# Kernel optimization log

Hardware: AMD Instinct MI355X
Metric: run time of the kernel (lower is better)

The kernel has to match this reference:

```python
import jax, jax.numpy as jnp
import numpy as np

NEG_SLOPE = 0.2

def setup_inputs() -> dict:
    key = jax.random.key(0)
    k1, k2, k3 = jax.random.split(key, 3)
    B, C, H, W = 8, 256, 128, 128
    R = 16  # reduction -> squeeze dim C // R = 16
    Cs = C // R
    x = jax.random.normal(k1, (B, C, H, W), dtype=jnp.float32)
    w1 = jax.random.normal(k2, (Cs, C), dtype=jnp.float32) * (1.0 / np.sqrt(C))
    b1 = jnp.zeros((Cs,), dtype=jnp.float32)
    w2 = jax.random.normal(k3, (C, Cs), dtype=jnp.float32) * (1.0 / np.sqrt(Cs))
    b2 = jnp.zeros((C,), dtype=jnp.float32)
    return {"x": x, "w1": w1, "b1": b1, "w2": w2, "b2": b2}

def reference(x, w1, b1, w2, b2):
    # Global average pool over spatial dims: [B,C,H,W] -> [B,C]
    y = jnp.mean(x, axis=(2, 3))
    # 1x1 conv on [B,C,1,1] == GEMV: squeeze + LeakyReLU(0.2)
    y1 = jnp.einsum('bc,sc->bs', y, w1) + b1
    y1 = jnp.where(y1 >= 0, y1, NEG_SLOPE * y1)
    # excite + sigmoid gate
    y2 = jax.nn.sigmoid(jnp.einsum('bs,cs->bc', y1, w2) + b2)
    # broadcast channel-wise scale
    return x * y2[:, :, None, None]
```

## Files before the change

### kernel.cpp

```cpp
#include <hip/hip_runtime.h>
#include <math.h>


#define Bn 8
#define Cn 256
#define CSn 16
#define HWn 16384
#define HW4 4096
#define NEG_SLOPE 0.2f

__global__ __launch_bounds__(256) void pool_kernel(const float* __restrict__ x,
                                                   float* __restrict__ y) {
    const int bc = blockIdx.x;
    const float4* xp = (const float4*)(x + (size_t)bc * HWn);
    float sum = 0.f;
    #pragma unroll
    for (int i = 0; i < HW4 / 256; ++i) {
        float4 v = xp[threadIdx.x + i * 256];
        sum += (v.x + v.y) + (v.z + v.w);
    }
    #pragma unroll
    for (int off = 32; off > 0; off >>= 1)
        sum += __shfl_down(sum, off, 64);
    __shared__ float smem[4];
    const int lane = threadIdx.x & 63, wid = threadIdx.x >> 6;
    if (lane == 0) smem[wid] = sum;
    __syncthreads();
    if (threadIdx.x == 0) {
        float t = (smem[0] + smem[1]) + (smem[2] + smem[3]);
        y[bc] = t * (1.0f / (float)HWn);
    }
}

__global__ __launch_bounds__(256) void gate_kernel(const float* __restrict__ y,
                                                   const float* __restrict__ w1,
                                                   const float* __restrict__ b1,
                                                   const float* __restrict__ w2,
                                                   const float* __restrict__ b2,
                                                   float* __restrict__ y2) {
    __shared__ float y1s[Bn * CSn];
    const int t = threadIdx.x;
    if (t < Bn * CSn) {
        const int b = t / CSn, s = t % CSn;
        float acc = b1[s];
        const float* yb = y + b * Cn;
        const float* ws = w1 + s * Cn;
        #pragma unroll 8
        for (int c = 0; c < Cn; ++c) acc += yb[c] * ws[c];
        y1s[t] = (acc >= 0.f) ? acc : NEG_SLOPE * acc;
    }
    __syncthreads();
    const int c = t;
    const float* w2c = w2 + c * CSn;
    float bias = b2[c];
    #pragma unroll
    for (int b = 0; b < Bn; ++b) {
        float acc = bias;
        #pragma unroll
        for (int s = 0; s < CSn; ++s) acc += y1s[b * CSn + s] * w2c[s];
        y2[b * Cn + c] = 1.0f / (1.0f + __expf(-acc));
    }
}

__global__ __launch_bounds__(256) void scale_kernel(const float* __restrict__ x,
                                                    const float* __restrict__ y2,
                                                    float* __restrict__ out) {
    const size_t i = (size_t)blockIdx.x * 256 + threadIdx.x;
    const int bc = (int)(i >> 12);
    const float g = y2[bc];
    float4 v = ((const float4*)x)[i];
    v.x *= g; v.y *= g; v.z *= g; v.w *= g;
    ((float4*)out)[i] = v;
}

extern "C" void kernel_launch(void* const* d_in, const int* in_sizes, int n_in,
                              void* d_out, int out_size, void* d_ws, size_t ws_size,
                              hipStream_t stream) {
    const float* x  = (const float*)d_in[0];
    const float* w1 = (const float*)d_in[1];
    const float* b1 = (const float*)d_in[2];
    const float* w2 = (const float*)d_in[3];
    const float* b2 = (const float*)d_in[4];
    float* out = (float*)d_out;

    float* y  = (float*)d_ws;
    float* y2 = (float*)d_ws + Bn * Cn;

    pool_kernel<<<Bn * Cn, 256, 0, stream>>>(x, y);
    gate_kernel<<<1, 256, 0, stream>>>(y, w1, b1, w2, b2, y2);
    scale_kernel<<<(Bn * Cn * HWn / 4) / 256, 256, 0, stream>>>(x, y2, out);
}
```

Measured before the change: 265.8 us.

## Fuse pool, gate and scale into one cooperative kernel with grid sync

Replaces the three separate launches with one cooperative kernel of 1024 blocks. Each block pools two channel planes, then waits at a grid-wide sync. It then recomputes its batch's squeeze GEMV locally and scales the same two planes it just read, hoping to hit cache on the re-read. This removes two launch boundaries and the single-block gate kernel. In exchange it adds a grid barrier, redundant squeeze work in every block, and depends on all blocks being co-resident.

```diff
diff --git a/kernel.cpp b/kernel.cpp
--- a/kernel.cpp
+++ b/kernel.cpp
@@ -1,76 +1,94 @@
 #include <hip/hip_runtime.h>
+#include <hip/hip_cooperative_groups.h>
 #include <math.h>
 
+namespace cg = cooperative_groups;
 
 #define Bn 8
 #define Cn 256
 #define CSn 16
 #define HWn 16384
-#define HW4 4096
+#define PL4 4096
 #define NEG_SLOPE 0.2f
+#define NBLK 1024
 
-__global__ __launch_bounds__(256) void pool_kernel(const float* __restrict__ x,
-                                                   float* __restrict__ y) {
-    const int bc = blockIdx.x;
-    const float4* xp = (const float4*)(x + (size_t)bc * HWn);
-    float sum = 0.f;
-    #pragma unroll
-    for (int i = 0; i < HW4 / 256; ++i) {
-        float4 v = xp[threadIdx.x + i * 256];
-        sum += (v.x + v.y) + (v.z + v.w);
+__global__ __launch_bounds__(256, 4) void fused_kernel(
+    const float* __restrict__ x,  const float* __restrict__ w1,
+    const float* __restrict__ b1, const float* __restrict__ w2,
+    const float* __restrict__ b2, float* __restrict__ out,
+    float* __restrict__ y) {
+    const int t = threadIdx.x;
+    const int bc0 = blockIdx.x * 2;
+    const float4* p0 = (const float4*)x + (size_t)bc0 * PL4;
+    const float4* p1 = p0 + PL4;
+
+    float s0 = 0.f, s1 = 0.f;
+    #pragma unroll 4
+    for (int i = 0; i < PL4 / 256; ++i) {
+        float4 a = p0[t + i * 256];
+        float4 b = p1[t + i * 256];
+        s0 += (a.x + a.y) + (a.z + a.w);
+        s1 += (b.x + b.y) + (b.z + b.w);
     }
     #pragma unroll
-    for (int off = 32; off > 0; off >>= 1)
-        sum += __shfl_down(sum, off, 64);
-    __shared__ float smem[4];
-    const int lane = threadIdx.x & 63, wid = threadIdx.x >> 6;
-    if (lane == 0) smem[wid] = sum;
+    for (int off = 32; off; off >>= 1) {
+        s0 += __shfl_down(s0, off, 64);
+        s1 += __shfl_down(s1, off, 64);
+    }
+    __shared__ float sm0[4], sm1[4];
+    const int lane = t & 63, wid = t >> 6;
+    if (lane == 0) { sm0[wid] = s0; sm1[wid] = s1; }
     __syncthreads();
-    if (threadIdx.x == 0) {
-        float t = (smem[0] + smem[1]) + (smem[2] + smem[3]);
-        y[bc] = t * (1.0f / (float)HWn);
+    if (t == 0) {
+        y[bc0]     = (sm0[0] + sm0[1] + sm0[2] + sm0[3]) * (1.f / (float)HWn);
+        y[bc0 + 1] = (sm1[0] + sm1[1] + sm1[2] + sm1[3]) * (1.f / (float)HWn);
+        __threadfence();
     }
-}
 
-__global__ __launch_bounds__(256) void gate_kernel(const float* __restrict__ y,
-                                                   const float* __restrict__ w1,
-                                                   const float* __restrict__ b1,
-                                                   const float* __restrict__ w2,
-                                                   const float* __restrict__ b2,
-                                                   float* __restrict__ y2) {
-    __shared__ float y1s[Bn * CSn];
-    const int t = threadIdx.x;
-    if (t < Bn * CSn) {
-        const int b = t / CSn, s = t % CSn;
-        float acc = b1[s];
-        const float* yb = y + b * Cn;
-        const float* ws = w1 + s * Cn;
-        #pragma unroll 8
-        for (int c = 0; c < Cn; ++c) acc += yb[c] * ws[c];
+    cg::this_grid().sync();
+
+    const int b = bc0 >> 8;
+    __shared__ float part[16 * 17];
+    __shared__ float y1s[16];
+    __shared__ float gv[2];
+    {
+        const int s = t >> 4, j = t & 15;
+        const float* yb = y  + b * Cn + j * 16;
+        const float* wr = w1 + s * Cn + j * 16;
+        float p = 0.f;
+        #pragma unroll
+        for (int k = 0; k < 16; ++k) p += yb[k] * wr[k];
+        part[s * 17 + j] = p;
+    }
+    __syncthreads();
+    if (t < 16) {
+        float acc = b1[t];
+        #pragma unroll
+        for (int j = 0; j < 16; ++j) acc += part[t * 17 + j];
         y1s[t] = (acc >= 0.f) ? acc : NEG_SLOPE * acc;
     }
     __syncthreads();
-    const int c = t;
-    const float* w2c = w2 + c * CSn;
-    float bias = b2[c];
-    #pragma unroll
-    for (int b = 0; b < Bn; ++b) {
-        float acc = bias;
+    if (t < 2) {
+        const int c = (bc0 + t) & (Cn - 1);
+        float acc = b2[c];
         #pragma unroll
-        for (int s = 0; s < CSn; ++s) acc += y1s[b * CSn + s] * w2c[s];
-        y2[b * Cn + c] = 1.0f / (1.0f + __expf(-acc));
+        for (int s = 0; s < CSn; ++s) acc += y1s[s] * w2[c * CSn + s];
+        gv[t] = 1.f / (1.f + __expf(-acc));
     }
-}
+    __syncthreads();
+    const float g0 = gv[0], g1 = gv[1];
 
-__global__ __launch_bounds__(256) void scale_kernel(const float* __restrict__ x,
-                                                    const float* __restrict__ y2,
-                                                    float* __restrict__ out) {
-    const size_t i = (size_t)blockIdx.x * 256 + threadIdx.x;
-    const int bc = (int)(i >> 12);
-    const float g = y2[bc];
-    float4 v = ((const float4*)x)[i];
-    v.x *= g; v.y *= g; v.z *= g; v.w *= g;
-    ((float4*)out)[i] = v;
+    float4* o0 = (float4*)out + (size_t)bc0 * PL4;
+    float4* o1 = o0 + PL4;
+    #pragma unroll 4
+    for (int i = 0; i < PL4 / 256; ++i) {
+        float4 a  = p0[t + i * 256];
+        float4 b4 = p1[t + i * 256];
+        a.x *= g0;  a.y *= g0;  a.z *= g0;  a.w *= g0;
+        b4.x *= g1; b4.y *= g1; b4.z *= g1; b4.w *= g1;
+        o0[t + i * 256] = a;
+        o1[t + i * 256] = b4;
+    }
 }
 
 extern "C" void kernel_launch(void* const* d_in, const int* in_sizes, int n_in,
@@ -82,11 +100,10 @@
     const float* w2 = (const float*)d_in[3];
     const float* b2 = (const float*)d_in[4];
     float* out = (float*)d_out;
+    float* y   = (float*)d_ws;
 
-    float* y  = (float*)d_ws;
-    float* y2 = (float*)d_ws + Bn * Cn;
-
-    pool_kernel<<<Bn * Cn, 256, 0, stream>>>(x, y);
-    gate_kernel<<<1, 256, 0, stream>>>(y, w1, b1, w2, b2, y2);
-    scale_kernel<<<(Bn * Cn * HWn / 4) / 256, 256, 0, stream>>>(x, y2, out);
+    void* args[] = {(void*)&x, (void*)&w1, (void*)&b1, (void*)&w2,
+                    (void*)&b2, (void*)&out, (void*)&y};
+    hipLaunchCooperativeKernel((void*)fused_kernel, dim3(NBLK), dim3(256),
+                               args, 0, stream);
 }
```

Measured after the change: 413.5 us. 1.56x slower.

## Fuse gate computation into scale kernel with per-channel blocks and nontemporal stores

Applied to the files above, without the earlier changes.

Removes the single-block gate kernel and instead has each scale block, one per (batch, channel) plane, recompute the squeeze GEMV, LeakyReLU and its own sigmoid gate from the pooled means. The scale kernel now loops over a full 16384-element plane per block and writes the output with nontemporal stores. This drops one launch and the serial one-block gate stage, at the cost of redundant small GEMV work in every block and fewer, larger blocks.

```diff
diff --git a/kernel.cpp b/kernel.cpp
--- a/kernel.cpp
+++ b/kernel.cpp
@@ -1,76 +1,84 @@
 #include <hip/hip_runtime.h>
 #include <math.h>
-
 
 #define Bn 8
 #define Cn 256
 #define CSn 16
 #define HWn 16384
-#define HW4 4096
+#define PL4 4096
 #define NEG_SLOPE 0.2f
+
+typedef float f4v __attribute__((ext_vector_type(4)));
 
 __global__ __launch_bounds__(256) void pool_kernel(const float* __restrict__ x,
                                                    float* __restrict__ y) {
     const int bc = blockIdx.x;
-    const float4* xp = (const float4*)(x + (size_t)bc * HWn);
+    const f4v* xp = (const f4v*)x + (size_t)bc * PL4;
+    const int t = threadIdx.x;
     float sum = 0.f;
     #pragma unroll
-    for (int i = 0; i < HW4 / 256; ++i) {
-        float4 v = xp[threadIdx.x + i * 256];
+    for (int i = 0; i < 16; ++i) {
+        f4v v = xp[t + i * 256];
         sum += (v.x + v.y) + (v.z + v.w);
     }
     #pragma unroll
-    for (int off = 32; off > 0; off >>= 1)
+    for (int off = 32; off; off >>= 1)
         sum += __shfl_down(sum, off, 64);
-    __shared__ float smem[4];
-    const int lane = threadIdx.x & 63, wid = threadIdx.x >> 6;
-    if (lane == 0) smem[wid] = sum;
+    __shared__ float sm[4];
+    if ((t & 63) == 0) sm[t >> 6] = sum;
     __syncthreads();
-    if (threadIdx.x == 0) {
-        float t = (smem[0] + smem[1]) + (smem[2] + smem[3]);
-        y[bc] = t * (1.0f / (float)HWn);
-    }
-}
-
-__global__ __launch_bounds__(256) void gate_kernel(const float* __restrict__ y,
-                                                   const float* __restrict__ w1,
-                                                   const float* __restrict__ b1,
-                                                   const float* __restrict__ w2,
-                                                   const float* __restrict__ b2,
-                                                   float* __restrict__ y2) {
-    __shared__ float y1s[Bn * CSn];
-    const int t = threadIdx.x;
-    if (t < Bn * CSn) {
-        const int b = t / CSn, s = t % CSn;
-        float acc = b1[s];
-        const float* yb = y + b * Cn;
-        const float* ws = w1 + s * Cn;
-        #pragma unroll 8
-        for (int c = 0; c < Cn; ++c) acc += yb[c] * ws[c];
-        y1s[t] = (acc >= 0.f) ? acc : NEG_SLOPE * acc;
-    }
-    __syncthreads();
-    const int c = t;
-    const float* w2c = w2 + c * CSn;
-    float bias = b2[c];
-    #pragma unroll
-    for (int b = 0; b < Bn; ++b) {
-        float acc = bias;
-        #pragma unroll
-        for (int s = 0; s < CSn; ++s) acc += y1s[b * CSn + s] * w2c[s];
-        y2[b * Cn + c] = 1.0f / (1.0f + __expf(-acc));
-    }
+    if (t == 0)
+        y[bc] = (sm[0] + sm[1] + sm[2] + sm[3]) * (1.f / (float)HWn);
 }
 
 __global__ __launch_bounds__(256) void scale_kernel(const float* __restrict__ x,
-                                                    const float* __restrict__ y2,
+                                                    const float* __restrict__ y,
+                                                    const float* __restrict__ w1,
+                                                    const float* __restrict__ b1,
+                                                    const float* __restrict__ w2,
+                                                    const float* __restrict__ b2,
                                                     float* __restrict__ out) {
-    const size_t i = (size_t)blockIdx.x * 256 + threadIdx.x;
-    const int bc = (int)(i >> 12);
-    const float g = y2[bc];
-    float4 v = ((const float4*)x)[i];
-    v.x *= g; v.y *= g; v.z *= g; v.w *= g;
-    ((float4*)out)[i] = v;
+    const int bc = blockIdx.x;
+    const int b = bc >> 8, c = bc & (Cn - 1);
+    const int t = threadIdx.x;
+
+    __shared__ float part[CSn * 17];
+    __shared__ float y1s[CSn];
+    __shared__ float gsh;
+    {
+        const int s = t >> 4, j = t & 15;
+        const float* yb = y  + b * Cn + j * 16;
+        const float* wr = w1 + s * Cn + j * 16;
+        float p = 0.f;
+        #pragma unroll
+        for (int k = 0; k < 16; ++k) p += yb[k] * wr[k];
+        part[s * 17 + j] = p;
+    }
+    __syncthreads();
+    if (t < CSn) {
+        float a = b1[t];
+        #pragma unroll
+        for (int j = 0; j < 16; ++j) a += part[t * 17 + j];
+        y1s[t] = (a >= 0.f) ? a : NEG_SLOPE * a;
+    }
+    __syncthreads();
+    if (t == 0) {
+        float a = b2[c];
+        #pragma unroll
+        for (int s = 0; s < CSn; ++s) a += y1s[s] * w2[c * CSn + s];
+        gsh = 1.f / (1.f + __expf(-a));
+    }
+    __syncthreads();
+    const float g = gsh;
+
+    const f4v* xp = (const f4v*)x + (size_t)bc * PL4;
+    f4v* op = (f4v*)out + (size_t)bc * PL4;
+    #pragma unroll
+    for (int i = 0; i < 16; ++i) {
+        f4v v = xp[t + i * 256];
+        v *= g;
+        __builtin_nontemporal_store(v, &op[t + i * 256]);
+    }
 }
 
 extern "C" void kernel_launch(void* const* d_in, const int* in_sizes, int n_in,
@@ -82,11 +90,8 @@
     const float* w2 = (const float*)d_in[3];
     const float* b2 = (const float*)d_in[4];
     float* out = (float*)d_out;
-
-    float* y  = (float*)d_ws;
-    float* y2 = (float*)d_ws + Bn * Cn;
+    float* y   = (float*)d_ws;
 
     pool_kernel<<<Bn * Cn, 256, 0, stream>>>(x, y);
-    gate_kernel<<<1, 256, 0, stream>>>(y, w1, b1, w2, b2, y2);
-    scale_kernel<<<(Bn * Cn * HWn / 4) / 256, 256, 0, stream>>>(x, y2, out);
+    scale_kernel<<<Bn * Cn, 256, 0, stream>>>(x, y, w1, b1, w2, b2, out);
 }
```

Result: faster. 258.2 us (-2.9%).
